# Performance work log

Hardware: AMD Instinct MI355X
Metric: run time of the kernel (lower is better)

The kernel has to match this reference:

```python
import jax, jax.numpy as jnp
import numpy as np

B, S, H = 64, 2048, 512


def _xavier(key, shape):
    fan_in, fan_out = shape[-1], shape[-2] if len(shape) > 1 else 1
    limit = float(np.sqrt(6.0 / (fan_in + fan_out)))
    return jax.random.uniform(key, shape, jnp.float32, -limit, limit)


def setup_inputs() -> dict:
    key = jax.random.key(0)
    k1, k2, k3, k4, k5, k6 = jax.random.split(key, 6)
    keys_ = jax.random.normal(k1, (B, S, H), jnp.float32)
    query = jax.random.normal(k2, (B, H), jnp.float32)
    v1 = _xavier(k3, (H,))
    W1 = _xavier(k4, (H, 2 * H))
    v2 = _xavier(k5, (H,))
    W2 = _xavier(k6, (H, 2 * H))
    return {"keys": keys_, "query": query, "v1": v1, "W1": W1, "v2": v2, "W2": W2}


def reference(keys, query, v1, W1, v2, W2):
    b, s, h = keys.shape
    # Stage 1: additive (Bahdanau) scoring over concat(keys, broadcast query)
    q = jnp.broadcast_to(query[:, None, :], (b, s, h))          # [B,S,H]
    hidden = jnp.concatenate([keys, q], axis=2)                  # [B,S,2H]
    t1 = jnp.tanh(jnp.einsum('de,bse->bsd', W1, hidden))         # [B,S,H]
    scores = jnp.einsum('d,bsd->bs', v1, t1)                     # [B,S]
    attns = jax.nn.softmax(scores, axis=1)                       # [B,S]
    # values == keys in the original module
    new_q = jnp.einsum('bs,bsh->bh', attns, keys)                # [B,H]
    # Stage 2: score again against concat(keys, broadcast new_query)
    nq = jnp.broadcast_to(new_q[:, None, :], (b, s, h))
    hidden2 = jnp.concatenate([keys, nq], axis=2)                # [B,S,2H]
    t2 = jnp.tanh(jnp.einsum('de,bse->bsd', W2, hidden2))        # [B,S,H]
    attn_vecs = jnp.einsum('d,bsd->bs', v2, t2)[:, None, :]      # [B,1,S]
    return attn_vecs
```

## Files before the change

kernel.cpp:

```cpp
#include <hip/hip_runtime.h>
#include <cstdint>
#include <cstddef>

#define S_DIM 2048

typedef __attribute__((ext_vector_type(8))) short short8;
typedef __attribute__((ext_vector_type(4))) float f32x4;

static __device__ __forceinline__ unsigned short f2bf(float f) {
  union { float f; unsigned int u; } v; v.f = f;
  unsigned int r = (v.u + 0x7fffu + ((v.u >> 16) & 1u)) >> 16;
  return (unsigned short)r;
}

static __device__ __forceinline__ float bf2f(unsigned short u) {
  union { unsigned int u; float f; } v; v.u = ((unsigned int)u) << 16;
  return v.f;
}

static __device__ __forceinline__ float fast_tanh(float x) {
  x = fminf(15.f, fmaxf(-15.f, x));
  float e = __expf(x + x);
  return 1.f - 2.f * __builtin_amdgcn_rcpf(e + 1.f);
}

static __device__ __forceinline__ void gload_lds16(const void* g, void* l) {
  __builtin_amdgcn_global_load_lds(
      (const __attribute__((address_space(1))) void*)g,
      (__attribute__((address_space(3))) void*)l, 16, 0, 0);
}


__global__ __launch_bounds__(256) void pack_b_kernel(
    const float* __restrict__ W1, const float* __restrict__ W2,
    unsigned short* __restrict__ wkp1, unsigned short* __restrict__ wkp2) {
  int j = blockIdx.x * 256 + threadIdx.x;
  const float* W = (j < 32768) ? W1 : W2;
  unsigned short* o = (j < 32768) ? wkp1 : wkp2;
  int wt = j & 32767;
  int k0 = wt >> 11, g = (wt >> 6) & 31, lhi = (wt >> 4) & 3, l15 = wt & 15;
  const float* src = W + (size_t)(g * 16 + l15) * 1024 + k0 * 32 + lhi * 8;
  float4 f0 = *reinterpret_cast<const float4*>(src);
  float4 f1 = *reinterpret_cast<const float4*>(src + 4);
  short8 hv;
  hv[0] = (short)f2bf(f0.x); hv[1] = (short)f2bf(f0.y);
  hv[2] = (short)f2bf(f0.z); hv[3] = (short)f2bf(f0.w);
  hv[4] = (short)f2bf(f1.x); hv[5] = (short)f2bf(f1.y);
  hv[6] = (short)f2bf(f1.z); hv[7] = (short)f2bf(f1.w);
  *reinterpret_cast<short8*>(o + (size_t)wt * 8) = hv;
}

__global__ __launch_bounds__(512, 4) void fused_pack_scores_kernel(
    const float* __restrict__ keys, const unsigned short* __restrict__ wkp,
    const float* __restrict__ v, const float* __restrict__ qp,
    unsigned short* __restrict__ akp, float* __restrict__ out) {
  __shared__ __align__(16) unsigned short lds_a[32768];
  __shared__ float lds_score[8][64];

  const int tid  = threadIdx.x;
  const int wid  = tid >> 6;
  const int lane = tid & 63;
  const int l15  = lane & 15;
  const int lhi  = lane >> 4;
  const int tile = blockIdx.x;
  const int row0 = tile * 64;
  const int b    = row0 >> 11;
  const int wcol = wid * 64;

  {
    const int s_mr  = (tid >> 6) & 3;
    const int s_lhi = (tid >> 4) & 3;
    const int s_l15 = tid & 15;
    const int k0_0  = tid >> 8;
    const float* srow =
        keys + (size_t)(row0 + s_mr * 16 + s_l15) * 512 + s_lhi * 8;
    unsigned short* atile = akp + (size_t)tile * 32768;
    #pragma unroll
    for (int i = 0; i < 8; ++i) {
      const int c  = i * 512 + tid;
      const int k0 = k0_0 + 2 * i;
      const float* src = srow + k0 * 32;
      float4 f0 = *reinterpret_cast<const float4*>(src);
      float4 f1 = *reinterpret_cast<const float4*>(src + 4);
      short8 hv;
      hv[0] = (short)f2bf(f0.x); hv[1] = (short)f2bf(f0.y);
      hv[2] = (short)f2bf(f0.z); hv[3] = (short)f2bf(f0.w);
      hv[4] = (short)f2bf(f1.x); hv[5] = (short)f2bf(f1.y);
      hv[6] = (short)f2bf(f1.z); hv[7] = (short)f2bf(f1.w);
      *reinterpret_cast<short8*>((char*)lds_a + c * 16) = hv;
      *reinterpret_cast<short8*>(atile + (size_t)c * 8) = hv;
    }
  }

  const unsigned short* wbase = wkp + (size_t)wid * 2048 + (size_t)lane * 8;
  short8 bb[2][4];
  #pragma unroll
  for (int nc = 0; nc < 4; ++nc)
    bb[0][nc] = *reinterpret_cast<const short8*>(wbase + nc * 512);

  __syncthreads();

  f32x4 acc[4][4];
  #pragma unroll
  for (int mr = 0; mr < 4; ++mr)
    #pragma unroll
    for (int nc = 0; nc < 4; ++nc) {
      f32x4 z = {0.f, 0.f, 0.f, 0.f};
      acc[mr][nc] = z;
    }

  const char* abase = (const char*)lds_a + lane * 16;

  #pragma unroll
  for (int k0 = 0; k0 < 16; ++k0) {
    const int cur = k0 & 1, nxt = cur ^ 1;
    if (k0 < 15) {
      #pragma unroll
      for (int nc = 0; nc < 4; ++nc)
        bb[nxt][nc] = *reinterpret_cast<const short8*>(
            wbase + (size_t)(k0 + 1) * 16384 + nc * 512);
    }
    short8 a[4];
    #pragma unroll
    for (int mr = 0; mr < 4; ++mr)
      a[mr] = *reinterpret_cast<const short8*>(abase + k0 * 4096 + mr * 1024);
    #pragma unroll
    for (int mr = 0; mr < 4; ++mr)
      #pragma unroll
      for (int nc = 0; nc < 4; ++nc)
        acc[mr][nc] = __builtin_amdgcn_mfma_f32_16x16x32_bf16(
            a[mr], bb[cur][nc], acc[mr][nc], 0, 0, 0);
  }

  float rp[4][4];
  #pragma unroll
  for (int mr = 0; mr < 4; ++mr)
    #pragma unroll
    for (int j = 0; j < 4; ++j) rp[mr][j] = 0.f;

  #pragma unroll
  for (int nc = 0; nc < 4; ++nc) {
    int col = wcol + nc * 16 + l15;
    float vv = v[col];
    float qv = qp[b * 512 + col];
    #pragma unroll
    for (int mr = 0; mr < 4; ++mr)
      #pragma unroll
      for (int j = 0; j < 4; ++j)
        rp[mr][j] += fast_tanh(acc[mr][nc][j] + qv) * vv;
  }

  #pragma unroll
  for (int off = 1; off < 16; off <<= 1)
    #pragma unroll
    for (int mr = 0; mr < 4; ++mr)
      #pragma unroll
      for (int j = 0; j < 4; ++j)
        rp[mr][j] += __shfl_xor(rp[mr][j], off, 64);

  if (l15 == 0) {
    #pragma unroll
    for (int mr = 0; mr < 4; ++mr)
      #pragma unroll
      for (int j = 0; j < 4; ++j)
        lds_score[wid][mr * 16 + lhi * 4 + j] = rp[mr][j];
  }
  __syncthreads();
  if (tid < 64) {
    float s = 0.f;
    #pragma unroll
    for (int w = 0; w < 8; ++w) s += lds_score[w][tid];
    out[row0 + tid] = s;
  }
}

__global__ __launch_bounds__(512, 4) void fused_packed_kernel(
    const unsigned short* __restrict__ akp, const unsigned short* __restrict__ wkp,
    const float* __restrict__ v, const float* __restrict__ qp,
    float* __restrict__ out) {
  __shared__ __align__(16) unsigned short lds_a[32768];
  __shared__ float lds_score[8][64];

  const int tid  = threadIdx.x;
  const int wid  = tid >> 6;
  const int lane = tid & 63;
  const int l15  = lane & 15;
  const int lhi  = lane >> 4;
  const int tile = blockIdx.x;
  const int row0 = tile * 64;
  const int b    = row0 >> 11;
  const int wcol = wid * 64;

  const unsigned short* atile = akp + (size_t)tile * 32768;
  #pragma unroll
  for (int i = 0; i < 8; ++i)
    gload_lds16(atile + (i * 512 + tid) * 8, (char*)lds_a + (i * 512 + tid) * 16);

  const unsigned short* wbase = wkp + (size_t)wid * 2048 + (size_t)lane * 8;
  short8 bb[2][4];
  #pragma unroll
  for (int nc = 0; nc < 4; ++nc)
    bb[0][nc] = *reinterpret_cast<const short8*>(wbase + nc * 512);

  __syncthreads();

  f32x4 acc[4][4];
  #pragma unroll
  for (int mr = 0; mr < 4; ++mr)
    #pragma unroll
    for (int nc = 0; nc < 4; ++nc) {
      f32x4 z = {0.f, 0.f, 0.f, 0.f};
      acc[mr][nc] = z;
    }

  const char* abase = (const char*)lds_a + lane * 16;

  #pragma unroll
  for (int k0 = 0; k0 < 16; ++k0) {
    const int cur = k0 & 1, nxt = cur ^ 1;
    if (k0 < 15) {
      #pragma unroll
      for (int nc = 0; nc < 4; ++nc)
        bb[nxt][nc] = *reinterpret_cast<const short8*>(
            wbase + (size_t)(k0 + 1) * 16384 + nc * 512);
    }
    short8 a[4];
    #pragma unroll
    for (int mr = 0; mr < 4; ++mr)
      a[mr] = *reinterpret_cast<const short8*>(abase + k0 * 4096 + mr * 1024);
    #pragma unroll
    for (int mr = 0; mr < 4; ++mr)
      #pragma unroll
      for (int nc = 0; nc < 4; ++nc)
        acc[mr][nc] = __builtin_amdgcn_mfma_f32_16x16x32_bf16(
            a[mr], bb[cur][nc], acc[mr][nc], 0, 0, 0);
  }

  float rp[4][4];
  #pragma unroll
  for (int mr = 0; mr < 4; ++mr)
    #pragma unroll
    for (int j = 0; j < 4; ++j) rp[mr][j] = 0.f;

  #pragma unroll
  for (int nc = 0; nc < 4; ++nc) {
    int col = wcol + nc * 16 + l15;
    float vv = v[col];
    float qv = qp[b * 512 + col];
    #pragma unroll
    for (int mr = 0; mr < 4; ++mr)
      #pragma unroll
      for (int j = 0; j < 4; ++j)
        rp[mr][j] += fast_tanh(acc[mr][nc][j] + qv) * vv;
  }

  #pragma unroll
  for (int off = 1; off < 16; off <<= 1)
    #pragma unroll
    for (int mr = 0; mr < 4; ++mr)
      #pragma unroll
      for (int j = 0; j < 4; ++j)
        rp[mr][j] += __shfl_xor(rp[mr][j], off, 64);

  if (l15 == 0) {
    #pragma unroll
    for (int mr = 0; mr < 4; ++mr)
      #pragma unroll
      for (int j = 0; j < 4; ++j)
        lds_score[wid][mr * 16 + lhi * 4 + j] = rp[mr][j];
  }
  __syncthreads();
  if (tid < 64) {
    float s = 0.f;
    #pragma unroll
    for (int w = 0; w < 8; ++w) s += lds_score[w][tid];
    out[row0 + tid] = s;
  }
}

__global__ __launch_bounds__(256) void wsum_packed_kernel(
    const unsigned short* __restrict__ akp, const float* __restrict__ attn,
    float* __restrict__ new_q) {
  int b = blockIdx.x, k0 = blockIdx.y;
  int t = threadIdx.x;
  int mr = t >> 6, lhi = (t >> 4) & 3, l15 = t & 15;
  const unsigned short* base =
      akp + (size_t)b * 32 * 32768 + (size_t)k0 * 2048 + (size_t)t * 8;
  const float* ab = attn + b * S_DIM + mr * 16 + l15;
  float acc[8];
  #pragma unroll
  for (int e = 0; e < 8; ++e) acc[e] = 0.f;
  #pragma unroll 4
  for (int tile = 0; tile < 32; ++tile) {
    short8 kv = *reinterpret_cast<const short8*>(base + (size_t)tile * 32768);
    float w = ab[tile * 64];
    #pragma unroll
    for (int e = 0; e < 8; ++e)
      acc[e] += w * bf2f((unsigned short)kv[e]);
  }
  __shared__ float red[4][64][8];
  #pragma unroll
  for (int e = 0; e < 8; ++e) red[lhi][mr * 16 + l15][e] = acc[e];
  __syncthreads();
  if (t < 32) {
    int lh = t >> 3, e = t & 7;
    float s = 0.f;
    #pragma unroll 8
    for (int r = 0; r < 64; ++r) s += red[lh][r][e];
    new_q[b * 512 + k0 * 32 + lh * 8 + e] = s;
  }
}


__global__ __launch_bounds__(512) void qproj_kernel(
    const float* __restrict__ W, const float* __restrict__ x,
    float* __restrict__ qp) {
  __shared__ float xs[512];
  int b = blockIdx.x, d = threadIdx.x;
  xs[d] = x[b * 512 + d];
  __syncthreads();
  const float4* wr = (const float4*)(W + (size_t)d * 1024 + 512);
  const float4* xv = (const float4*)xs;
  float acc = 0.f;
  #pragma unroll 8
  for (int h = 0; h < 128; ++h) {
    float4 w4 = wr[h], x4 = xv[h];
    acc += w4.x * x4.x + w4.y * x4.y + w4.z * x4.z + w4.w * x4.w;
  }
  qp[b * 512 + d] = acc;
}

__global__ __launch_bounds__(256) void softmax_kernel(float* __restrict__ sc) {
  int b = blockIdx.x, tid = threadIdx.x;
  float* row = sc + (size_t)b * S_DIM;
  float vv[8];
  float m = -1e30f;
  #pragma unroll
  for (int i = 0; i < 8; ++i) { vv[i] = row[tid + i * 256]; m = fmaxf(m, vv[i]); }
  #pragma unroll
  for (int off = 32; off; off >>= 1) m = fmaxf(m, __shfl_xor(m, off, 64));
  __shared__ float red[4], red2[4];
  int wid = tid >> 6, lane = tid & 63;
  if (lane == 0) red[wid] = m;
  __syncthreads();
  m = fmaxf(fmaxf(red[0], red[1]), fmaxf(red[2], red[3]));
  float s = 0.f;
  #pragma unroll
  for (int i = 0; i < 8; ++i) { vv[i] = __expf(vv[i] - m); s += vv[i]; }
  #pragma unroll
  for (int off = 32; off; off >>= 1) s += __shfl_xor(s, off, 64);
  if (lane == 0) red2[wid] = s;
  __syncthreads();
  s = red2[0] + red2[1] + red2[2] + red2[3];
  float inv = 1.f / s;
  #pragma unroll
  for (int i = 0; i < 8; ++i) row[tid + i * 256] = vv[i] * inv;
}


__global__ __launch_bounds__(256) void convw_kernel(
    const float* __restrict__ W1, const float* __restrict__ W2,
    unsigned short* __restrict__ wk1, unsigned short* __restrict__ wk2) {
  int idx = blockIdx.x * 256 + threadIdx.x;
  const float* W = (idx < 262144) ? W1 : W2;
  unsigned short* o = (idx < 262144) ? wk1 : wk2;
  int j = idx & 262143;
  int d = j >> 9, h = j & 511;
  o[j] = f2bf(W[(size_t)d * 1024 + h]);
}

__global__ __launch_bounds__(512, 4) void fused_scores_kernel(
    const float* __restrict__ keys, const unsigned short* __restrict__ wk,
    const float* __restrict__ v, const float* __restrict__ qp,
    float* __restrict__ out) {
  __shared__ __align__(16) unsigned short lds_k[64 * 512];
  __shared__ float lds_score[8][64];
  char* lds_b = (char*)lds_k;
  const int tid  = threadIdx.x;
  const int wid  = tid >> 6;
  const int lane = tid & 63;
  const int l15  = lane & 15;
  const int lhi  = lane >> 4;
  const int row0 = blockIdx.x * 64;
  const int b    = row0 >> 11;
  const int wcol = wid * 64;
  #pragma unroll
  for (int i = 0; i < 8; ++i) {
    int c = i * 512 + tid;
    int r = c >> 6, k = (c & 63) * 8;
    const float* src = keys + (size_t)(row0 + r) * 512 + k;
    const float4 f0 = *reinterpret_cast<const float4*>(src);
    const float4 f1 = *reinterpret_cast<const float4*>(src + 4);
    short8 hv;
    hv[0] = (short)f2bf(f0.x); hv[1] = (short)f2bf(f0.y);
    hv[2] = (short)f2bf(f0.z); hv[3] = (short)f2bf(f0.w);
    hv[4] = (short)f2bf(f1.x); hv[5] = (short)f2bf(f1.y);
    hv[6] = (short)f2bf(f1.z); hv[7] = (short)f2bf(f1.w);
    int byte = (r * 1024 + k * 2) ^ ((r & 7) << 4);
    *reinterpret_cast<short8*>(lds_b + byte) = hv;
  }
  __syncthreads();
  f32x4 acc[4][4];
  #pragma unroll
  for (int mr = 0; mr < 4; ++mr)
    #pragma unroll
    for (int nc = 0; nc < 4; ++nc) {
      f32x4 z = {0.f, 0.f, 0.f, 0.f};
      acc[mr][nc] = z;
    }
  const int koff = lhi * 8;
  #pragma unroll 1
  for (int k0 = 0; k0 < 512; k0 += 32) {
    short8 a[4], bbv[4];
    #pragma unroll
    for (int nc = 0; nc < 4; ++nc) {
      const unsigned short* p =
          wk + (((size_t)(wcol + nc * 16 + l15)) << 9) + k0 + koff;
      bbv[nc] = *reinterpret_cast<const short8*>(p);
    }
    #pragma unroll
    for (int mr = 0; mr < 4; ++mr) {
      int r = mr * 16 + l15;
      int byte = (r * 1024 + (k0 + koff) * 2) ^ ((r & 7) << 4);
      a[mr] = *reinterpret_cast<const short8*>(lds_b + byte);
    }
    #pragma unroll
    for (int mr = 0; mr < 4; ++mr)
      #pragma unroll
      for (int nc = 0; nc < 4; ++nc)
        acc[mr][nc] = __builtin_amdgcn_mfma_f32_16x16x32_bf16(
            a[mr], bbv[nc], acc[mr][nc], 0, 0, 0);
  }
  float rp[4][4];
  #pragma unroll
  for (int mr = 0; mr < 4; ++mr)
    #pragma unroll
    for (int j = 0; j < 4; ++j) rp[mr][j] = 0.f;
  #pragma unroll
  for (int nc = 0; nc < 4; ++nc) {
    int col = wcol + nc * 16 + l15;
    float vv = v[col];
    float qv = qp[b * 512 + col];
    #pragma unroll
    for (int mr = 0; mr < 4; ++mr)
      #pragma unroll
      for (int j = 0; j < 4; ++j)
        rp[mr][j] += fast_tanh(acc[mr][nc][j] + qv) * vv;
  }
  #pragma unroll
  for (int off = 1; off < 16; off <<= 1)
    #pragma unroll
    for (int mr = 0; mr < 4; ++mr)
      #pragma unroll
      for (int j = 0; j < 4; ++j)
        rp[mr][j] += __shfl_xor(rp[mr][j], off, 64);
  if (l15 == 0) {
    #pragma unroll
    for (int mr = 0; mr < 4; ++mr)
      #pragma unroll
      for (int j = 0; j < 4; ++j)
        lds_score[wid][mr * 16 + lhi * 4 + j] = rp[mr][j];
  }
  __syncthreads();
  if (tid < 64) {
    float s = 0.f;
    #pragma unroll
    for (int w = 0; w < 8; ++w) s += lds_score[w][tid];
    out[row0 + tid] = s;
  }
}

__global__ __launch_bounds__(512) void wsum_part_kernel(
    const float* __restrict__ keys, const float* __restrict__ attn,
    float* __restrict__ part) {
  int b = blockIdx.x, sc = blockIdx.y;
  int tid = threadIdx.x;
  int c4 = tid & 127, rg = tid >> 7;
  const float* kb = keys + ((size_t)(b * S_DIM + sc * 128 + rg * 32)) * 512 + c4 * 4;
  const float* ab = attn + b * S_DIM + sc * 128 + rg * 32;
  float4 acc = {0.f, 0.f, 0.f, 0.f};
  #pragma unroll 8
  for (int i = 0; i < 32; ++i) {
    float w = ab[i];
    float4 kv = *reinterpret_cast<const float4*>(kb + (size_t)i * 512);
    acc.x += w * kv.x; acc.y += w * kv.y; acc.z += w * kv.z; acc.w += w * kv.w;
  }
  __shared__ float4 red[4][128];
  red[rg][c4] = acc;
  __syncthreads();
  if (tid < 128) {
    float4 a0 = red[0][tid], a1 = red[1][tid], a2 = red[2][tid], a3 = red[3][tid];
    float4 s;
    s.x = a0.x + a1.x + a2.x + a3.x;
    s.y = a0.y + a1.y + a2.y + a3.y;
    s.z = a0.z + a1.z + a2.z + a3.z;
    s.w = a0.w + a1.w + a2.w + a3.w;
    *reinterpret_cast<float4*>(part + ((size_t)b * 16 + sc) * 512 + tid * 4) = s;
  }
}

__global__ __launch_bounds__(512) void wsum_final_kernel(
    const float* __restrict__ part, float* __restrict__ new_q) {
  int b = blockIdx.x, h = threadIdx.x;
  float acc = 0.f;
  #pragma unroll
  for (int sc = 0; sc < 16; ++sc) acc += part[((size_t)b * 16 + sc) * 512 + h];
  new_q[b * 512 + h] = acc;
}


extern "C" void kernel_launch(void* const* d_in, const int* in_sizes, int n_in,
                              void* d_out, int out_size, void* d_ws, size_t ws_size,
                              hipStream_t stream) {
  (void)in_sizes; (void)n_in; (void)out_size;
  const float* keys  = (const float*)d_in[0];
  const float* query = (const float*)d_in[1];
  const float* v1    = (const float*)d_in[2];
  const float* W1    = (const float*)d_in[3];
  const float* v2    = (const float*)d_in[4];
  const float* W2    = (const float*)d_in[5];
  float* out = (float*)d_out;
  float* wsf = (float*)d_ws;

  const size_t FAST_NEED = 491520ull * 4ull + 67108864ull * 2ull;
  if (ws_size >= FAST_NEED) {
    float* qp1   = wsf;
    float* attn  = wsf + 32768;
    float* new_q = wsf + 163840;
    float* qp2   = wsf + 196608;
    unsigned short* wkp1 = (unsigned short*)(wsf + 229376);
    unsigned short* wkp2 = wkp1 + 262144;
    unsigned short* akp  = (unsigned short*)(wsf + 491520);

    pack_b_kernel<<<256, 256, 0, stream>>>(W1, W2, wkp1, wkp2);
    qproj_kernel<<<64, 512, 0, stream>>>(W1, query, qp1);
    fused_pack_scores_kernel<<<2048, 512, 0, stream>>>(keys, wkp1, v1, qp1, akp, attn);
    softmax_kernel<<<64, 256, 0, stream>>>(attn);
    wsum_packed_kernel<<<dim3(64, 16), 256, 0, stream>>>(akp, attn, new_q);
    qproj_kernel<<<64, 512, 0, stream>>>(W2, new_q, qp2);
    fused_packed_kernel<<<2048, 512, 0, stream>>>(akp, wkp2, v2, qp2, out);
  } else {
    float* qp1   = wsf;
    float* attn  = wsf + 32768;
    float* new_q = wsf + 163840;
    float* qp2   = wsf + 196608;
    float* part  = wsf + 229376;
    unsigned short* wk1 = (unsigned short*)(wsf + 753664);
    unsigned short* wk2 = wk1 + 262144;

    convw_kernel<<<2048, 256, 0, stream>>>(W1, W2, wk1, wk2);
    qproj_kernel<<<64, 512, 0, stream>>>(W1, query, qp1);
    fused_scores_kernel<<<2048, 512, 0, stream>>>(keys, wk1, v1, qp1, attn);
    softmax_kernel<<<64, 256, 0, stream>>>(attn);
    wsum_part_kernel<<<dim3(64, 16), 512, 0, stream>>>(keys, attn, part);
    wsum_final_kernel<<<64, 512, 0, stream>>>(part, new_q);
    qproj_kernel<<<64, 512, 0, stream>>>(W2, new_q, qp2);
    fused_scores_kernel<<<2048, 512, 0, stream>>>(keys, wk2, v2, qp2, out);
  }
}
```

Before: 303.2 us.

## Double M-tile to 128 rows per block with split-K LDS double buffering

Both scoring kernels now process 128 rows per block instead of 64, so each wave's W fragments feed twice as many MFMAs. This halves the global weight traffic per row. The K dimension is split into two halves held in separate LDS buffers, so the second half's key load (and pack) overlaps MFMA work on the first half. The cost is 64KB+ of LDS and 128 accumulator registers per thread, which lowers occupancy from 4 to 2 blocks per CU.

```diff
diff --git a/kernel.cpp b/kernel.cpp
--- a/kernel.cpp
+++ b/kernel.cpp
@@ -50,227 +50,283 @@
   *reinterpret_cast<short8*>(o + (size_t)wt * 8) = hv;
 }
 
-__global__ __launch_bounds__(512, 4) void fused_pack_scores_kernel(
+__global__ __launch_bounds__(512, 2) void fused_pack_scores128_kernel(
     const float* __restrict__ keys, const unsigned short* __restrict__ wkp,
     const float* __restrict__ v, const float* __restrict__ qp,
-    unsigned short* __restrict__ akp, float* __restrict__ out) {
-  __shared__ __align__(16) unsigned short lds_a[32768];
-  __shared__ float lds_score[8][64];
+    unsigned short* __restrict__ akp, float* __restrict__ scores1) {
+  __shared__ __align__(16) unsigned short lds_a[2][32768];
+  __shared__ float lds_score[8][128];
 
   const int tid  = threadIdx.x;
   const int wid  = tid >> 6;
   const int lane = tid & 63;
   const int l15  = lane & 15;
   const int lhi  = lane >> 4;
-  const int tile = blockIdx.x;
-  const int row0 = tile * 64;
+  const int blk  = blockIdx.x;
+  const int row0 = blk * 128;
   const int b    = row0 >> 11;
+  const int t64  = blk * 2;
   const int wcol = wid * 64;
 
+  const int sub   = tid & 255;
+  const int mr_s  = sub >> 6;
+  const int lhi_s = (sub >> 4) & 3;
+  const int l15_s = sub & 15;
+  const int k0b   = tid >> 8;
+  const int rowA  = row0 + mr_s * 16 + l15_s;
+
+  const unsigned short* wbase = wkp + (size_t)wid * 2048 + (size_t)lane * 8;
+
+#define S1_WRITE_CHUNK(I, HK)                                                  \
+  {                                                                            \
+    const int Tp_  = (I) >> 2;                                                 \
+    const int k0l_ = ((I) * 2 + k0b) & 7;                                      \
+    const int c_   = (I) * 512 + tid;                                          \
+    short8 hv;                                                                 \
+    hv[0] = (short)f2bf(f[I][0].x); hv[1] = (short)f2bf(f[I][0].y);            \
+    hv[2] = (short)f2bf(f[I][0].z); hv[3] = (short)f2bf(f[I][0].w);            \
+    hv[4] = (short)f2bf(f[I][1].x); hv[5] = (short)f2bf(f[I][1].y);            \
+    hv[6] = (short)f2bf(f[I][1].z); hv[7] = (short)f2bf(f[I][1].w);            \
+    *reinterpret_cast<short8*>(&lds_a[HK][c_ * 8]) = hv;                       \
+    *reinterpret_cast<short8*>(                                                \
+        akp + (size_t)(t64 + Tp_) * 32768 +                                    \
+        ((size_t)((HK) * 8 + k0l_) * 256 + sub) * 8) = hv;                     \
+  }
+
   {
-    const int s_mr  = (tid >> 6) & 3;
-    const int s_lhi = (tid >> 4) & 3;
-    const int s_l15 = tid & 15;
-    const int k0_0  = tid >> 8;
-    const float* srow =
-        keys + (size_t)(row0 + s_mr * 16 + s_l15) * 512 + s_lhi * 8;
-    unsigned short* atile = akp + (size_t)tile * 32768;
+    float4 f[8][2];
     #pragma unroll
     for (int i = 0; i < 8; ++i) {
-      const int c  = i * 512 + tid;
-      const int k0 = k0_0 + 2 * i;
-      const float* src = srow + k0 * 32;
-      float4 f0 = *reinterpret_cast<const float4*>(src);
-      float4 f1 = *reinterpret_cast<const float4*>(src + 4);
-      short8 hv;
-      hv[0] = (short)f2bf(f0.x); hv[1] = (short)f2bf(f0.y);
-      hv[2] = (short)f2bf(f0.z); hv[3] = (short)f2bf(f0.w);
-      hv[4] = (short)f2bf(f1.x); hv[5] = (short)f2bf(f1.y);
-      hv[6] = (short)f2bf(f1.z); hv[7] = (short)f2bf(f1.w);
-      *reinterpret_cast<short8*>((char*)lds_a + c * 16) = hv;
-      *reinterpret_cast<short8*>(atile + (size_t)c * 8) = hv;
-    }
-  }
-
-  const unsigned short* wbase = wkp + (size_t)wid * 2048 + (size_t)lane * 8;
-  short8 bb[2][4];
-  #pragma unroll
-  for (int nc = 0; nc < 4; ++nc)
-    bb[0][nc] = *reinterpret_cast<const short8*>(wbase + nc * 512);
-
-  __syncthreads();
-
-  f32x4 acc[4][4];
-  #pragma unroll
-  for (int mr = 0; mr < 4; ++mr)
+      const int Tp  = i >> 2;
+      const int k0l = (i * 2 + k0b) & 7;
+      const float* src =
+          keys + (size_t)(rowA + Tp * 64) * 512 + k0l * 32 + lhi_s * 8;
+      f[i][0] = *reinterpret_cast<const float4*>(src);
+      f[i][1] = *reinterpret_cast<const float4*>(src + 4);
+    }
+    #pragma unroll
+    for (int i = 0; i < 8; ++i) S1_WRITE_CHUNK(i, 0)
+  }
+  __syncthreads();
+
+  f32x4 acc[8][4];
+  #pragma unroll
+  for (int mr2 = 0; mr2 < 8; ++mr2)
     #pragma unroll
     for (int nc = 0; nc < 4; ++nc) {
       f32x4 z = {0.f, 0.f, 0.f, 0.f};
-      acc[mr][nc] = z;
-    }
-
-  const char* abase = (const char*)lds_a + lane * 16;
-
-  #pragma unroll
-  for (int k0 = 0; k0 < 16; ++k0) {
-    const int cur = k0 & 1, nxt = cur ^ 1;
-    if (k0 < 15) {
+      acc[mr2][nc] = z;
+    }
+
+  {
+    float4 f[8][2];
+    #pragma unroll
+    for (int j = 0; j < 8; ++j) {
+      short8 bbv[4];
       #pragma unroll
       for (int nc = 0; nc < 4; ++nc)
-        bb[nxt][nc] = *reinterpret_cast<const short8*>(
-            wbase + (size_t)(k0 + 1) * 16384 + nc * 512);
-    }
-    short8 a[4];
-    #pragma unroll
-    for (int mr = 0; mr < 4; ++mr)
-      a[mr] = *reinterpret_cast<const short8*>(abase + k0 * 4096 + mr * 1024);
-    #pragma unroll
-    for (int mr = 0; mr < 4; ++mr)
+        bbv[nc] = *reinterpret_cast<const short8*>(
+            wbase + (size_t)j * 16384 + nc * 512);
+      {
+        const int Tp  = j >> 2;
+        const int k0l = (j * 2 + k0b) & 7;
+        const float* src =
+            keys + (size_t)(rowA + Tp * 64) * 512 + 256 + k0l * 32 + lhi_s * 8;
+        f[j][0] = *reinterpret_cast<const float4*>(src);
+        f[j][1] = *reinterpret_cast<const float4*>(src + 4);
+      }
+      #pragma unroll
+      for (int mr2 = 0; mr2 < 8; ++mr2) {
+        const short8 a = *reinterpret_cast<const short8*>(
+            &lds_a[0][((mr2 >> 2) * 2048 + j * 256 + (mr2 & 3) * 64 + lane) * 8]);
+        #pragma unroll
+        for (int nc = 0; nc < 4; ++nc)
+          acc[mr2][nc] = __builtin_amdgcn_mfma_f32_16x16x32_bf16(
+              a, bbv[nc], acc[mr2][nc], 0, 0, 0);
+      }
+      if (j >= 4) { const int i = j - 4; S1_WRITE_CHUNK(i, 1) }
+    }
+    #pragma unroll
+    for (int i = 4; i < 8; ++i) S1_WRITE_CHUNK(i, 1)
+  }
+  __syncthreads();
+
+  #pragma unroll
+  for (int j = 0; j < 8; ++j) {
+    short8 bbv[4];
+    #pragma unroll
+    for (int nc = 0; nc < 4; ++nc)
+      bbv[nc] = *reinterpret_cast<const short8*>(
+          wbase + (size_t)(8 + j) * 16384 + nc * 512);
+    #pragma unroll
+    for (int mr2 = 0; mr2 < 8; ++mr2) {
+      const short8 a = *reinterpret_cast<const short8*>(
+          &lds_a[1][((mr2 >> 2) * 2048 + j * 256 + (mr2 & 3) * 64 + lane) * 8]);
       #pragma unroll
       for (int nc = 0; nc < 4; ++nc)
-        acc[mr][nc] = __builtin_amdgcn_mfma_f32_16x16x32_bf16(
-            a[mr], bb[cur][nc], acc[mr][nc], 0, 0, 0);
-  }
-
-  float rp[4][4];
-  #pragma unroll
-  for (int mr = 0; mr < 4; ++mr)
-    #pragma unroll
-    for (int j = 0; j < 4; ++j) rp[mr][j] = 0.f;
-
+        acc[mr2][nc] = __builtin_amdgcn_mfma_f32_16x16x32_bf16(
+            a, bbv[nc], acc[mr2][nc], 0, 0, 0);
+    }
+  }
+
+  float rp[8][4];
+  #pragma unroll
+  for (int mr2 = 0; mr2 < 8; ++mr2)
+    #pragma unroll
+    for (int j = 0; j < 4; ++j) rp[mr2][j] = 0.f;
   #pragma unroll
   for (int nc = 0; nc < 4; ++nc) {
-    int col = wcol + nc * 16 + l15;
-    float vv = v[col];
-    float qv = qp[b * 512 + col];
-    #pragma unroll
-    for (int mr = 0; mr < 4; ++mr)
-      #pragma unroll
-      for (int j = 0; j < 4; ++j)
-        rp[mr][j] += fast_tanh(acc[mr][nc][j] + qv) * vv;
-  }
-
+    const int col = wcol + nc * 16 + l15;
+    const float vv = v[col];
+    const float qv = qp[b * 512 + col];
+    #pragma unroll
+    for (int mr2 = 0; mr2 < 8; ++mr2)
+      #pragma unroll
+      for (int j = 0; j < 4; ++j)
+        rp[mr2][j] += fast_tanh(acc[mr2][nc][j] + qv) * vv;
+  }
   #pragma unroll
   for (int off = 1; off < 16; off <<= 1)
     #pragma unroll
-    for (int mr = 0; mr < 4; ++mr)
-      #pragma unroll
-      for (int j = 0; j < 4; ++j)
-        rp[mr][j] += __shfl_xor(rp[mr][j], off, 64);
-
+    for (int mr2 = 0; mr2 < 8; ++mr2)
+      #pragma unroll
+      for (int j = 0; j < 4; ++j)
+        rp[mr2][j] += __shfl_xor(rp[mr2][j], off, 64);
   if (l15 == 0) {
     #pragma unroll
-    for (int mr = 0; mr < 4; ++mr)
-      #pragma unroll
-      for (int j = 0; j < 4; ++j)
-        lds_score[wid][mr * 16 + lhi * 4 + j] = rp[mr][j];
-  }
-  __syncthreads();
-  if (tid < 64) {
+    for (int mr2 = 0; mr2 < 8; ++mr2)
+      #pragma unroll
+      for (int j = 0; j < 4; ++j)
+        lds_score[wid][mr2 * 16 + lhi * 4 + j] = rp[mr2][j];
+  }
+  __syncthreads();
+  if (tid < 128) {
     float s = 0.f;
     #pragma unroll
     for (int w = 0; w < 8; ++w) s += lds_score[w][tid];
-    out[row0 + tid] = s;
-  }
-}
-
-__global__ __launch_bounds__(512, 4) void fused_packed_kernel(
+    scores1[row0 + tid] = s;
+  }
+#undef S1_WRITE_CHUNK
+}
+
+__global__ __launch_bounds__(512, 2) void fused_packed128_kernel(
     const unsigned short* __restrict__ akp, const unsigned short* __restrict__ wkp,
     const float* __restrict__ v, const float* __restrict__ qp,
     float* __restrict__ out) {
-  __shared__ __align__(16) unsigned short lds_a[32768];
-  __shared__ float lds_score[8][64];
+  __shared__ __align__(16) unsigned short lds_a[2][32768];
+  __shared__ float lds_score[8][128];
 
   const int tid  = threadIdx.x;
   const int wid  = tid >> 6;
   const int lane = tid & 63;
   const int l15  = lane & 15;
   const int lhi  = lane >> 4;
-  const int tile = blockIdx.x;
-  const int row0 = tile * 64;
+  const int blk  = blockIdx.x;
+  const int row0 = blk * 128;
   const int b    = row0 >> 11;
+  const int t64  = blk * 2;
   const int wcol = wid * 64;
 
-  const unsigned short* atile = akp + (size_t)tile * 32768;
-  #pragma unroll
-  for (int i = 0; i < 8; ++i)
-    gload_lds16(atile + (i * 512 + tid) * 8, (char*)lds_a + (i * 512 + tid) * 16);
-
+  const int sub = tid & 255;
+  const int k0b = tid >> 8;
+  const unsigned short* at = akp + (size_t)t64 * 32768;
   const unsigned short* wbase = wkp + (size_t)wid * 2048 + (size_t)lane * 8;
-  short8 bb[2][4];
-  #pragma unroll
-  for (int nc = 0; nc < 4; ++nc)
-    bb[0][nc] = *reinterpret_cast<const short8*>(wbase + nc * 512);
-
-  __syncthreads();
-
-  f32x4 acc[4][4];
-  #pragma unroll
-  for (int mr = 0; mr < 4; ++mr)
+
+  #pragma unroll
+  for (int i = 0; i < 8; ++i) {
+    const int Tp  = i >> 2;
+    const int k0l = (i * 2 + k0b) & 7;
+    const int c   = i * 512 + tid;
+    gload_lds16(at + (size_t)Tp * 32768 + ((size_t)k0l * 256 + sub) * 8,
+                (char*)&lds_a[0][0] + c * 16);
+  }
+  __syncthreads();
+
+  f32x4 acc[8][4];
+  #pragma unroll
+  for (int mr2 = 0; mr2 < 8; ++mr2)
     #pragma unroll
     for (int nc = 0; nc < 4; ++nc) {
       f32x4 z = {0.f, 0.f, 0.f, 0.f};
-      acc[mr][nc] = z;
-    }
-
-  const char* abase = (const char*)lds_a + lane * 16;
-
-  #pragma unroll
-  for (int k0 = 0; k0 < 16; ++k0) {
-    const int cur = k0 & 1, nxt = cur ^ 1;
-    if (k0 < 15) {
+      acc[mr2][nc] = z;
+    }
+
+  #pragma unroll
+  for (int j = 0; j < 8; ++j) {
+    short8 bbv[4];
+    #pragma unroll
+    for (int nc = 0; nc < 4; ++nc)
+      bbv[nc] = *reinterpret_cast<const short8*>(
+          wbase + (size_t)j * 16384 + nc * 512);
+    {
+      const int Tp  = j >> 2;
+      const int k0l = (j * 2 + k0b) & 7;
+      const int c   = j * 512 + tid;
+      gload_lds16(at + (size_t)Tp * 32768 + ((size_t)(8 + k0l) * 256 + sub) * 8,
+                  (char*)&lds_a[1][0] + c * 16);
+    }
+    #pragma unroll
+    for (int mr2 = 0; mr2 < 8; ++mr2) {
+      const short8 a = *reinterpret_cast<const short8*>(
+          &lds_a[0][((mr2 >> 2) * 2048 + j * 256 + (mr2 & 3) * 64 + lane) * 8]);
       #pragma unroll
       for (int nc = 0; nc < 4; ++nc)
-        bb[nxt][nc] = *reinterpret_cast<const short8*>(
-            wbase + (size_t)(k0 + 1) * 16384 + nc * 512);
-    }
-    short8 a[4];
-    #pragma unroll
-    for (int mr = 0; mr < 4; ++mr)
-      a[mr] = *reinterpret_cast<const short8*>(abase + k0 * 4096 + mr * 1024);
-    #pragma unroll
-    for (int mr = 0; mr < 4; ++mr)
+        acc[mr2][nc] = __builtin_amdgcn_mfma_f32_16x16x32_bf16(
+            a, bbv[nc], acc[mr2][nc], 0, 0, 0);
+    }
+  }
+  __syncthreads();
+
+  #pragma unroll
+  for (int j = 0; j < 8; ++j) {
+    short8 bbv[4];
+    #pragma unroll
+    for (int nc = 0; nc < 4; ++nc)
+      bbv[nc] = *reinterpret_cast<const short8*>(
+          wbase + (size_t)(8 + j) * 16384 + nc * 512);
+    #pragma unroll
+    for (int mr2 = 0; mr2 < 8; ++mr2) {
+      const short8 a = *reinterpret_cast<const short8*>(
+          &lds_a[1][((mr2 >> 2) * 2048 + j * 256 + (mr2 & 3) * 64 + lane) * 8]);
       #pragma unroll
       for (int nc = 0; nc < 4; ++nc)
-        acc[mr][nc] = __builtin_amdgcn_mfma_f32_16x16x32_bf16(
-            a[mr], bb[cur][nc], acc[mr][nc], 0, 0, 0);
-  }
-
-  float rp[4][4];
-  #pragma unroll
-  for (int mr = 0; mr < 4; ++mr)
-    #pragma unroll
-    for (int j = 0; j < 4; ++j) rp[mr][j] = 0.f;
-
+        acc[mr2][nc] = __builtin_amdgcn_mfma_f32_16x16x32_bf16(
+            a, bbv[nc], acc[mr2][nc], 0, 0, 0);
+    }
+  }
+
+  float rp[8][4];
+  #pragma unroll
+  for (int mr2 = 0; mr2 < 8; ++mr2)
+    #pragma unroll
+    for (int j = 0; j < 4; ++j) rp[mr2][j] = 0.f;
   #pragma unroll
   for (int nc = 0; nc < 4; ++nc) {
-    int col = wcol + nc * 16 + l15;
-    float vv = v[col];
-    float qv = qp[b * 512 + col];
-    #pragma unroll
-    for (int mr = 0; mr < 4; ++mr)
-      #pragma unroll
-      for (int j = 0; j < 4; ++j)
-        rp[mr][j] += fast_tanh(acc[mr][nc][j] + qv) * vv;
-  }
-
+    const int col = wcol + nc * 16 + l15;
+    const float vv = v[col];
+    const float qv = qp[b * 512 + col];
+    #pragma unroll
+    for (int mr2 = 0; mr2 < 8; ++mr2)
+      #pragma unroll
+      for (int j = 0; j < 4; ++j)
+        rp[mr2][j] += fast_tanh(acc[mr2][nc][j] + qv) * vv;
+  }
   #pragma unroll
   for (int off = 1; off < 16; off <<= 1)
     #pragma unroll
-    for (int mr = 0; mr < 4; ++mr)
-      #pragma unroll
-      for (int j = 0; j < 4; ++j)
-        rp[mr][j] += __shfl_xor(rp[mr][j], off, 64);
-
+    for (int mr2 = 0; mr2 < 8; ++mr2)
+      #pragma unroll
+      for (int j = 0; j < 4; ++j)
+        rp[mr2][j] += __shfl_xor(rp[mr2][j], off, 64);
   if (l15 == 0) {
     #pragma unroll
-    for (int mr = 0; mr < 4; ++mr)
-      #pragma unroll
-      for (int j = 0; j < 4; ++j)
-        lds_score[wid][mr * 16 + lhi * 4 + j] = rp[mr][j];
-  }
-  __syncthreads();
-  if (tid < 64) {
+    for (int mr2 = 0; mr2 < 8; ++mr2)
+      #pragma unroll
+      for (int j = 0; j < 4; ++j)
+        lds_score[wid][mr2 * 16 + lhi * 4 + j] = rp[mr2][j];
+  }
+  __syncthreads();
+  if (tid < 128) {
     float s = 0.f;
     #pragma unroll
     for (int w = 0; w < 8; ++w) s += lds_score[w][tid];
@@ -534,11 +590,12 @@
 
     pack_b_kernel<<<256, 256, 0, stream>>>(W1, W2, wkp1, wkp2);
     qproj_kernel<<<64, 512, 0, stream>>>(W1, query, qp1);
-    fused_pack_scores_kernel<<<2048, 512, 0, stream>>>(keys, wkp1, v1, qp1, akp, attn);
+    fused_pack_scores128_kernel<<<1024, 512, 0, stream>>>(
+        keys, wkp1, v1, qp1, akp, attn);
     softmax_kernel<<<64, 256, 0, stream>>>(attn);
     wsum_packed_kernel<<<dim3(64, 16), 256, 0, stream>>>(akp, attn, new_q);
     qproj_kernel<<<64, 512, 0, stream>>>(W2, new_q, qp2);
-    fused_packed_kernel<<<2048, 512, 0, stream>>>(akp, wkp2, v2, qp2, out);
+    fused_packed128_kernel<<<1024, 512, 0, stream>>>(akp, wkp2, v2, qp2, out);
   } else {
     float* qp1   = wsf;
     float* attn  = wsf + 32768;
```

Result: slower. 317.1 us (+4.6%).
